# Kernel tuning notes

Measured on AMD Instinct MI355X. Metric: run time of the kernel, lower is better.

The kernel has to match this reference:

```python
import jax, jax.numpy as jnp
import numpy as np

S, E, K, D = 50000, 20000, 128, 64
NUM_LAYER = 3
E1, E0 = 1000000, 1000000  # nnz of pos / neg adjacency
B = 4096


def _edges(key, n_rows, n_cols, n_edges):
    k1, k2, k3 = jax.random.split(key, 3)
    rows = jax.random.randint(k1, (n_edges,), 0, n_rows)
    cols = jax.random.randint(k2, (n_edges,), 0, n_cols)
    vals = jax.random.uniform(k3, (n_edges,), jnp.float32, 0.0, 0.1)
    return rows, cols, vals


def setup_inputs() -> dict:
    key = jax.random.key(0)
    ks = jax.random.split(key, 32)
    inp = {}
    inp['stu_id'] = jax.random.randint(ks[0], (B,), 0, S)
    inp['exer_id'] = jax.random.randint(ks[1], (B,), 0, E)
    inp['kn_emb'] = (jax.random.uniform(ks[2], (B, K)) < 0.1).astype(jnp.float32)
    # embeddings
    inp['stu_emb'] = jax.random.normal(ks[3], (S, D), jnp.float32) * 0.1
    inp['exer_emb'] = jax.random.normal(ks[4], (E, D), jnp.float32) * 0.1
    inp['kn_base'] = jax.random.normal(ks[5], (K, D), jnp.float32) * 0.1
    inp['stu_bias'] = jax.random.normal(ks[6], (S, 1), jnp.float32) * 0.1
    inp['e_disc'] = jax.random.normal(ks[7], (E, 1), jnp.float32) * 0.1
    # GCN linear layers
    inp['W1_w'] = jax.random.normal(ks[8], (K, K), jnp.float32) * (1.0 / np.sqrt(K))
    inp['W1_b'] = jnp.zeros((K,), jnp.float32)
    inp['W0_w'] = jax.random.normal(ks[9], (K, K), jnp.float32) * (1.0 / np.sqrt(K))
    inp['W0_b'] = jnp.zeros((K,), jnp.float32)
    # PosLinear prednet
    inp['pn1_w'] = jax.random.normal(ks[10], (256, K), jnp.float32) * 0.05
    inp['pn1_b'] = jnp.zeros((256,), jnp.float32)
    inp['pn2_w'] = jax.random.normal(ks[11], (128, 256), jnp.float32) * 0.05
    inp['pn2_b'] = jnp.zeros((128,), jnp.float32)
    inp['pn3_w'] = jax.random.normal(ks[12], (1, 128), jnp.float32) * 0.05
    inp['pn3_b'] = jnp.zeros((1,), jnp.float32)
    # sparse adjacencies (COO) pos(1) / neg(0), user->item and item->user
    r, c, v = _edges(ks[13], S, E, E1)
    inp['ui1_r'], inp['ui1_c'], inp['ui1_v'] = r, c, v
    r, c, v = _edges(ks[14], E, S, E1)
    inp['iu1_r'], inp['iu1_c'], inp['iu1_v'] = r, c, v
    r, c, v = _edges(ks[15], S, E, E0)
    inp['ui0_r'], inp['ui0_c'], inp['ui0_v'] = r, c, v
    r, c, v = _edges(ks[16], E, S, E0)
    inp['iu0_r'], inp['iu0_c'], inp['iu0_v'] = r, c, v
    # self-loop degree normalizers (1/(deg+1)-style positive scalars)
    inp['d_i_1'] = jax.random.uniform(ks[17], (S,), jnp.float32, 0.01, 1.0)
    inp['d_j_1'] = jax.random.uniform(ks[18], (E,), jnp.float32, 0.01, 1.0)
    inp['d_i_0'] = jax.random.uniform(ks[19], (S,), jnp.float32, 0.01, 1.0)
    inp['d_j_0'] = jax.random.uniform(ks[20], (E,), jnp.float32, 0.01, 1.0)
    return inp


def _spmm(rows, cols, vals, x, n_rows):
    # sparse [n_rows, n_cols] @ dense [n_cols, K]
    return jax.ops.segment_sum(vals[:, None] * x[cols], rows, num_segments=n_rows)


def _poslinear(x, w, b):
    wp = 2.0 * jax.nn.relu(-w) + w  # == |w|, as in PosLinear
    return x @ wp.T + b


def reference(stu_id, exer_id, kn_emb, stu_emb, exer_emb, kn_base, stu_bias, e_disc,
              W1_w, W1_b, W0_w, W0_b, pn1_w, pn1_b, pn2_w, pn2_b, pn3_w, pn3_b,
              ui1_r, ui1_c, ui1_v, iu1_r, iu1_c, iu1_v,
              ui0_r, ui0_c, ui0_v, iu0_r, iu0_c, iu0_v,
              d_i_1, d_j_1, d_i_0, d_j_0):
    # project embeddings onto knowledge space: [S,K], [E,K]
    stat = stu_emb @ kn_base.T
    kdiff = exer_emb @ kn_base.T
    for _ in range(NUM_LAYER):
        u1 = _spmm(ui1_r, ui1_c, ui1_v, kdiff, S) + stat * d_i_1[:, None]
        u1 = u1 @ W1_w.T + W1_b
        i1 = _spmm(iu1_r, iu1_c, iu1_v, stat, E) + kdiff * d_j_1[:, None]
        i1 = i1 @ W1_w.T + W1_b
        u0 = _spmm(ui0_r, ui0_c, ui0_v, kdiff, S) + stat * d_i_0[:, None]
        u0 = u0 @ W0_w.T + W0_b
        i0 = _spmm(iu0_r, iu0_c, iu0_v, stat, E) + kdiff * d_j_0[:, None]
        i0 = i0 @ W0_w.T + W0_b
        stat = u1 + u0
        kdiff = i1 + i0
    # diagnosis head (NCD-style), dropout in eval mode -> identity
    stat_b = jax.nn.sigmoid(stat[stu_id] + stu_bias[stu_id])      # [B,K]
    k_d = jax.nn.sigmoid(kdiff[exer_id])                           # [B,K]
    disc = jax.nn.sigmoid(e_disc[exer_id])                         # [B,1]
    x = disc * (stat_b - k_d) * kn_emb
    x = jax.nn.sigmoid(_poslinear(x, pn1_w, pn1_b))
    x = jax.nn.sigmoid(_poslinear(x, pn2_w, pn2_b))
    out = jax.nn.sigmoid(_poslinear(x, pn3_w, pn3_b)).reshape(-1)
    return out
```

## Files before the change

### kernel.cpp

```cpp
#include <hip/hip_runtime.h>
#include <hip/hip_bf16.h>

#define SN 50000
#define EN 20000
#define KN 128
#define DN 64
#define BN 4096
#define NE 1000000
#define NLAYER 3

#define CH_SHIFT 12
#define NCH0 5
#define NCH1 13
#define SIDE1_BASE2 (2 * SN * NCH0)
#define NTOT2 (2 * (SN * NCH0 + EN * NCH1))

#define BIN_SHIFT 11
#define NBIN2 ((NTOT2 + 2047) >> 11)
#define T1 4096
#define PG1 ((NE + T1 - 1) / T1)
#define HB 256

typedef float f32x4 __attribute__((ext_vector_type(4)));
typedef float f32x2 __attribute__((ext_vector_type(2)));
typedef short bf16x8 __attribute__((ext_vector_type(8)));

__device__ __forceinline__ float sigmoidf_(float v) { return 1.f / (1.f + __expf(-v)); }
__device__ __forceinline__ float bf_lo(unsigned u) { return __uint_as_float(u << 16); }
__device__ __forceinline__ float bf_hi(unsigned u) { return __uint_as_float(u & 0xffff0000u); }
__device__ __forceinline__ float bf_one(unsigned short s) { return __uint_as_float((unsigned)s << 16); }
__device__ __forceinline__ unsigned packbf2(float a, float b) {
    __hip_bfloat16 ha = __float2bfloat16(a), hb = __float2bfloat16(b);
    unsigned short ua = *(unsigned short*)&ha, ub = *(unsigned short*)&hb;
    return (unsigned)ua | ((unsigned)ub << 16);
}
__device__ __forceinline__ unsigned short packbf1(float a) {
    __hip_bfloat16 ha = __float2bfloat16(a);
    return *(unsigned short*)&ha;
}
__device__ __forceinline__ unsigned char fp8_of_bf16(unsigned short h) {
    float f = bf_one(h);
    int pk = __builtin_amdgcn_cvt_pk_fp8_f32(f, f, 0, false);
    return (unsigned char)(pk & 0xff);
}

struct CsrB {
    const int* rows[4]; const int* cols[4]; const float* vals[4];
};

__device__ __forceinline__ int bucket_idx(int a, int r, int cc) {
    int side = a >> 1;
    int nch = side ? NCH1 : NCH0;
    int base = side ? SIDE1_BASE2 : 0;
    int tb = a & 1;
    return base + (2 * r + tb) * nch + (cc >> CH_SHIFT);
}

__global__ __launch_bounds__(256) void hist_coarse(CsrB c, int* __restrict__ cnt) {
    __shared__ int h[512];
    const int t = threadIdx.x;
    h[t] = 0; h[t + 256] = 0;
    __syncthreads();
    const int a = blockIdx.x >> 8;
    const int tile = blockIdx.x & 255;
    const int per = (NE + HB - 1) / HB;
    const int beg = tile * per, end = min(beg + per, NE);
    for (int i = beg + t; i < end; i += 256)
        atomicAdd(&h[bucket_idx(a, c.rows[a][i], c.cols[a][i]) >> BIN_SHIFT], 1);
    __syncthreads();
    if (h[t]) atomicAdd(&cnt[t], h[t]);
    if (h[t + 256]) atomicAdd(&cnt[t + 256], h[t + 256]);
}

__global__ __launch_bounds__(512) void scan_coarse(const int* __restrict__ cnt,
                                                   int* __restrict__ base,
                                                   int* __restrict__ tails) {
    __shared__ int sh[512];
    const int t = threadIdx.x;
    const int v = (t < NBIN2) ? cnt[t] : 0;
    sh[t] = v;
    __syncthreads();
    for (int o = 1; o < 512; o <<= 1) {
        int x = sh[t]; int u = (t >= o) ? sh[t - o] : 0;
        __syncthreads(); sh[t] = x + u; __syncthreads();
    }
    if (t < NBIN2) {
        const int ex = sh[t] - v;
        base[t] = ex;
        tails[t] = ex;
    }
    if (t == 511) base[NBIN2] = sh[511];
}

__global__ __launch_bounds__(512) void part1(CsrB c, int* __restrict__ tails,
                                             int2* __restrict__ stg) {
    __shared__ int2 srec[T1];
    __shared__ unsigned short sbin[T1];
    __shared__ int h[512], offs[512], gbase[512], sc[512];
    const int t = threadIdx.x;
    const int a = blockIdx.x / PG1;
    const int tile = blockIdx.x - a * PG1;
    const int beg = tile * T1;
    const int cnt = min(T1, NE - beg);
    h[t] = 0;
    __syncthreads();

    int2 rec[8]; int rbin[8]; int rrank[8];
#pragma unroll
    for (int k = 0; k < 8; ++k) {
        int o = t + k * 512;
        if (o < cnt) {
            int i = beg + o;
            int cc = c.cols[a][i];
            int B = bucket_idx(a, c.rows[a][i], cc);
            int bin = B >> BIN_SHIFT;
            rec[k] = make_int2(cc | ((B & 2047) << 17), __float_as_int(c.vals[a][i]));
            rbin[k] = bin;
            rrank[k] = atomicAdd(&h[bin], 1);
        } else {
            rbin[k] = -1;
        }
    }
    __syncthreads();
    sc[t] = h[t];
    __syncthreads();
    for (int o = 1; o < 512; o <<= 1) {
        int x = sc[t]; int u = (t >= o) ? sc[t - o] : 0;
        __syncthreads(); sc[t] = x + u; __syncthreads();
    }
    offs[t] = sc[t] - h[t];
    if (h[t] > 0) gbase[t] = atomicAdd(&tails[t], h[t]);
    __syncthreads();
#pragma unroll
    for (int k = 0; k < 8; ++k) {
        if (rbin[k] >= 0) {
            int pos = offs[rbin[k]] + rrank[k];
            srec[pos] = rec[k];
            sbin[pos] = (unsigned short)rbin[k];
        }
    }
    __syncthreads();
    for (int idx = t; idx < cnt; idx += 512) {
        int b = sbin[idx];
        stg[gbase[b] + (idx - offs[b])] = srec[idx];
    }
}

__global__ __launch_bounds__(512) void part2(const int* __restrict__ coarseBase,
                                             const int2* __restrict__ stg,
                                             int* __restrict__ rp,
                                             int2* __restrict__ cv) {
    __shared__ int cnt2[2048];
    __shared__ int tsum[512];
    const int b = blockIdx.x;
    const int t = threadIdx.x;
    const int fineBase = b << BIN_SHIFT;
    const int nf = min(2048, NTOT2 - fineBase);
    const int segBeg = coarseBase[b];
    const int segEnd = coarseBase[b + 1];
    for (int i = t; i < 2048; i += 512) cnt2[i] = 0;
    __syncthreads();
    for (int e = segBeg + t; e < segEnd; e += 512)
        atomicAdd(&cnt2[((unsigned)stg[e].x) >> 17], 1);
    __syncthreads();
    const int i4 = t * 4;
    int v0 = cnt2[i4], v1 = cnt2[i4 + 1], v2 = cnt2[i4 + 2], v3 = cnt2[i4 + 3];
    tsum[t] = v0 + v1 + v2 + v3;
    __syncthreads();
    for (int o = 1; o < 512; o <<= 1) {
        int x = tsum[t]; int u = (t >= o) ? tsum[t - o] : 0;
        __syncthreads(); tsum[t] = x + u; __syncthreads();
    }
    const int pre = (t == 0) ? 0 : tsum[t - 1];
    const int p0 = pre, p1 = pre + v0, p2 = p1 + v1, p3 = p2 + v2;
    cnt2[i4] = p0; cnt2[i4 + 1] = p1; cnt2[i4 + 2] = p2; cnt2[i4 + 3] = p3;
    if (i4 + 0 < nf) rp[fineBase + i4 + 0] = segBeg + p0;
    if (i4 + 1 < nf) rp[fineBase + i4 + 1] = segBeg + p1;
    if (i4 + 2 < nf) rp[fineBase + i4 + 2] = segBeg + p2;
    if (i4 + 3 < nf) rp[fineBase + i4 + 3] = segBeg + p3;
    if (b == NBIN2 - 1 && t == 511) rp[NTOT2] = segEnd;
    __syncthreads();
    for (int e = segBeg + t; e < segEnd; e += 512) {
        int2 r = stg[e];
        int pos = segBeg + atomicAdd(&cnt2[((unsigned)r.x) >> 17], 1);
        cv[pos] = make_int2(r.x & 0xFFFF, r.y);
    }
}

__global__ __launch_bounds__(256) void f2bf3(
    const float* __restrict__ s0, unsigned short* __restrict__ d0, int n0,
    const float* __restrict__ s1, unsigned short* __restrict__ d1, int n1,
    const float* __restrict__ s2, unsigned short* __restrict__ d2, int n2) {
    int j = blockIdx.x * 256 + threadIdx.x;
    const float* s; unsigned short* d;
    if (j < n0) { s = s0; d = d0; }
    else {
        j -= n0;
        if (j < n1) { s = s1; d = d1; }
        else {
            j -= n1;
            if (j >= n2) return;
            s = s2; d = d2;
        }
    }
    float2 f = ((const float2*)s)[j];
    ((unsigned*)d)[j] = packbf2(f.x, f.y);
}

template <int KK>
__global__ __launch_bounds__(256) void gemm_proj(const float* __restrict__ X,
                                                 const unsigned short* __restrict__ W,
                                                 unsigned short* __restrict__ out,
                                                 unsigned char* __restrict__ f8,
                                                 int M) {
    constexpr int PITCH = KK + 8;
    __shared__ unsigned short Wl[128 * PITCH];
    const int t = threadIdx.x;
    for (int idx = t * 8; idx < 128 * KK; idx += 2048) {
        int r = idx / KK, k = idx - r * KK;
        *(uint4*)(&Wl[r * PITCH + k]) = *(const uint4*)(&W[idx]);
    }
    __syncthreads();
    const int lane = t & 63;
    const int nm = lane & 15;
    const int quad = lane >> 4;
    const int row0 = blockIdx.x * 64 + (t >> 6) * 16;
    if (row0 >= M) return;

    f32x4 acc[8];
#pragma unroll
    for (int nt = 0; nt < 8; ++nt) acc[nt] = (f32x4){0.f, 0.f, 0.f, 0.f};

    const float* xrow = X + (size_t)(row0 + nm) * KK + quad * 8;
#pragma unroll
    for (int ks = 0; ks < KK / 32; ++ks) {
        float4 f0 = *(const float4*)(xrow + ks * 32);
        float4 f1 = *(const float4*)(xrow + ks * 32 + 4);
        unsigned q[4] = {packbf2(f0.x, f0.y), packbf2(f0.z, f0.w),
                         packbf2(f1.x, f1.y), packbf2(f1.z, f1.w)};
        bf16x8 a = *(bf16x8*)q;
#pragma unroll
        for (int nt = 0; nt < 8; ++nt) {
            bf16x8 b = *(const bf16x8*)(&Wl[(nt * 16 + nm) * PITCH + ks * 32 + quad * 8]);
            acc[nt] = __builtin_amdgcn_mfma_f32_16x16x32_bf16(a, b, acc[nt], 0, 0, 0);
        }
    }
    const size_t obase = (size_t)(row0 + quad * 4) * 128 + nm;
    unsigned short* orow = out + obase;
    unsigned char* frow = f8 + obase;
#pragma unroll
    for (int r = 0; r < 4; ++r)
#pragma unroll
        for (int nt = 0; nt < 8; ++nt) {
            unsigned short h = packbf1(acc[nt][r]);
            orow[(size_t)r * 128 + nt * 16] = h;
            frow[(size_t)r * 128 + nt * 16] = fp8_of_bf16(h);
        }
}

template <bool LIST>
__global__ __launch_bounds__(512) void gemm2_mfma(
    const unsigned short* __restrict__ agg1S, const unsigned short* __restrict__ agg0S,
    const unsigned short* __restrict__ yS,
    const float* __restrict__ d1S, const float* __restrict__ d0S,
    unsigned short* __restrict__ outS, unsigned char* __restrict__ f8S,
    const unsigned short* __restrict__ agg1E, const unsigned short* __restrict__ agg0E,
    const unsigned short* __restrict__ yE,
    const float* __restrict__ d1E, const float* __restrict__ d0E,
    unsigned short* __restrict__ outE, unsigned char* __restrict__ f8E,
    const unsigned short* __restrict__ W1, const unsigned short* __restrict__ W0,
    const float* __restrict__ b1, const float* __restrict__ b0,
    const int* __restrict__ idsS, const int* __restrict__ idsE, int nblkS) {
    constexpr int PITCH = 136;
    __shared__ unsigned short Wl[2 * 128 * PITCH];
    const int t = threadIdx.x;
    for (int idx = t * 8; idx < 128 * 128; idx += 4096) {
        int r = idx >> 7, k = idx & 127;
        *(uint4*)(&Wl[r * PITCH + k]) = *(const uint4*)(&W1[idx]);
        *(uint4*)(&Wl[128 * PITCH + r * PITCH + k]) = *(const uint4*)(&W0[idx]);
    }
    __syncthreads();
    const bool sideE = (int)blockIdx.x >= nblkS;
    const unsigned short* agg1 = sideE ? agg1E : agg1S;
    const unsigned short* agg0 = sideE ? agg0E : agg0S;
    const unsigned short* y    = sideE ? yE : yS;
    const float* d1 = sideE ? d1E : d1S;
    const float* d0 = sideE ? d0E : d0S;
    unsigned short* out = sideE ? outE : outS;
    unsigned char* f8 = sideE ? f8E : f8S;
    const int M = LIST ? BN : (sideE ? EN : SN);
    const int lane = t & 63;
    const int nm = lane & 15;
    const int quad = lane >> 4;
    const int row0 = ((int)blockIdx.x - (sideE ? nblkS : 0)) * 128 + (t >> 6) * 16;
    if (row0 >= M) return;

    const int lrow = row0 + nm;
    int grow = lrow;
    if (LIST) grow = (sideE ? idsE : idsS)[lrow];

    const float d1v = d1[grow];
    const float d0v = d0[grow];

    f32x4 acc[8];
#pragma unroll
    for (int nt = 0; nt < 8; ++nt) acc[nt] = (f32x4){0.f, 0.f, 0.f, 0.f};

    const size_t rbA = (size_t)lrow * 128 + quad * 8;
    const size_t rbY = (size_t)grow * 128 + quad * 8;
#pragma unroll
    for (int ks = 0; ks < 4; ++ks) {
        uint4 ua1 = *(const uint4*)(agg1 + rbA + ks * 32);
        uint4 ua0 = *(const uint4*)(agg0 + rbA + ks * 32);
        uint4 uy  = *(const uint4*)(y    + rbY + ks * 32);
        uint4 p1, p0;
        {
            unsigned* a1 = (unsigned*)&ua1; unsigned* a0 = (unsigned*)&ua0;
            unsigned* yy = (unsigned*)&uy;
            unsigned* q1 = (unsigned*)&p1; unsigned* q0 = (unsigned*)&p0;
#pragma unroll
            for (int w = 0; w < 4; ++w) {
                float ylo = bf_lo(yy[w]), yhi = bf_hi(yy[w]);
                q1[w] = packbf2(bf_lo(a1[w]) + d1v * ylo, bf_hi(a1[w]) + d1v * yhi);
                q0[w] = packbf2(bf_lo(a0[w]) + d0v * ylo, bf_hi(a0[w]) + d0v * yhi);
            }
        }
        bf16x8 af1 = *(bf16x8*)&p1;
        bf16x8 af0 = *(bf16x8*)&p0;
#pragma unroll
        for (int nt = 0; nt < 8; ++nt) {
            bf16x8 bw1 = *(const bf16x8*)(&Wl[(nt * 16 + nm) * PITCH + ks * 32 + quad * 8]);
            acc[nt] = __builtin_amdgcn_mfma_f32_16x16x32_bf16(af1, bw1, acc[nt], 0, 0, 0);
            bf16x8 bw0 = *(const bf16x8*)(&Wl[128 * PITCH + (nt * 16 + nm) * PITCH + ks * 32 + quad * 8]);
            acc[nt] = __builtin_amdgcn_mfma_f32_16x16x32_bf16(af0, bw0, acc[nt], 0, 0, 0);
        }
    }
    const size_t obase = (size_t)(row0 + quad * 4) * 128 + nm;
    unsigned short* orow = out + obase;
    unsigned char* frow = f8 + obase;
#pragma unroll
    for (int nt = 0; nt < 8; ++nt) {
        float bb = b1[nt * 16 + nm] + b0[nt * 16 + nm];
#pragma unroll
        for (int r = 0; r < 4; ++r) {
            unsigned short h = packbf1(acc[nt][r] + bb);
            orow[(size_t)r * 128 + nt * 16] = h;
            if (!LIST) frow[(size_t)r * 128 + nt * 16] = fp8_of_bf16(h);
        }
    }
}

template <bool LIST>
__global__ __launch_bounds__(256) void spmm_all(
    const int* __restrict__ rp, const long long* __restrict__ cv,
    const unsigned char* __restrict__ kd8, const unsigned char* __restrict__ st8,
    unsigned short* __restrict__ as1, unsigned short* __restrict__ as0,
    unsigned short* __restrict__ ae1, unsigned short* __restrict__ ae0,
    const int* __restrict__ idsS, const int* __restrict__ idsE) {
    const int wave = (blockIdx.x * 256 + threadIdx.x) >> 6;
    const int lane = threadIdx.x & 63;
    const int NW = LIST ? 2 * BN : SN + EN;
    if (wave >= NW) return;
    const bool sideE = LIST ? (wave >= BN) : (wave >= SN);
    const int li = sideE ? (wave - (LIST ? BN : SN)) : wave;
    const int r = LIST ? (sideE ? idsE[li] : idsS[li]) : li;
    const int nch = sideE ? NCH1 : NCH0;
    const int* rpb = rp + (sideE ? SIDE1_BASE2 : 0);
    const int o = lane >> 3;
    const int c = lane & 7;
    const unsigned char* g8 = (sideE ? st8 : kd8) + c * 16;

    const int rbase = 2 * r * nch;
    const int e0 = rpb[rbase];
    const int em = rpb[rbase + nch];
    const int ee = rpb[rbase + 2 * nch];

    f32x2 acc[8];

#define OCT(E)                                                              \
    {                                                                       \
        int col = (int)((E) & 0xFFFF);                                      \
        float v = __int_as_float((int)((E) >> 32));                         \
        f32x2 vv = {v, v};                                                  \
        uint4 u = *(const uint4*)(g8 + (col << 7));                         \
        acc[0] += vv * __builtin_amdgcn_cvt_pk_f32_fp8((int)u.x, false);    \
        acc[1] += vv * __builtin_amdgcn_cvt_pk_f32_fp8((int)u.x, true);     \
        acc[2] += vv * __builtin_amdgcn_cvt_pk_f32_fp8((int)u.y, false);    \
        acc[3] += vv * __builtin_amdgcn_cvt_pk_f32_fp8((int)u.y, true);     \
        acc[4] += vv * __builtin_amdgcn_cvt_pk_f32_fp8((int)u.z, false);    \
        acc[5] += vv * __builtin_amdgcn_cvt_pk_f32_fp8((int)u.z, true);     \
        acc[6] += vv * __builtin_amdgcn_cvt_pk_f32_fp8((int)u.w, false);    \
        acc[7] += vv * __builtin_amdgcn_cvt_pk_f32_fp8((int)u.w, true);     \
    }

#define PHASE(EBEG, EEND)                                                   \
    {                                                                       \
        int e = (EBEG);                                                     \
        for (; e + 16 <= (EEND); e += 16) {                                 \
            long long E0 = cv[e + o];                                       \
            long long E1 = cv[e + 8 + o];                                   \
            OCT(E0) OCT(E1)                                                 \
        }                                                                   \
        for (; e + 8 <= (EEND); e += 8) {                                   \
            long long E0 = cv[e + o];                                       \
            OCT(E0)                                                         \
        }                                                                   \
        if (e < (EEND)) {                                                   \
            int idx = min(e + o, (EEND) - 1);                               \
            long long E0 = cv[idx];                                         \
            if (e + o >= (EEND)) E0 &= 0xFFFFLL;    \
            OCT(E0)                                                         \
        }                                                                   \
    }

#define REDUCE8                                                             \
    _Pragma("unroll")                                                       \
    for (int j = 0; j < 8; ++j) {                                           \
        acc[j].x += __shfl_xor(acc[j].x, 8);                                \
        acc[j].y += __shfl_xor(acc[j].y, 8);                                \
        acc[j].x += __shfl_xor(acc[j].x, 16);                               \
        acc[j].y += __shfl_xor(acc[j].y, 16);                               \
        acc[j].x += __shfl_xor(acc[j].x, 32);                               \
        acc[j].y += __shfl_xor(acc[j].y, 32);                               \
    }

    const int oi = LIST ? li : r;
    const int base = (oi << 7) + c * 16;
    unsigned short* o1 = sideE ? ae1 : as1;
    unsigned short* o0 = sideE ? ae0 : as0;

#pragma unroll
    for (int j = 0; j < 8; ++j) acc[j] = (f32x2){0.f, 0.f};
    PHASE(e0, em)
    REDUCE8
    if (o == 0) {
        uint4 w1, w2;
        w1.x = packbf2(acc[0].x, acc[0].y); w1.y = packbf2(acc[1].x, acc[1].y);
        w1.z = packbf2(acc[2].x, acc[2].y); w1.w = packbf2(acc[3].x, acc[3].y);
        w2.x = packbf2(acc[4].x, acc[4].y); w2.y = packbf2(acc[5].x, acc[5].y);
        w2.z = packbf2(acc[6].x, acc[6].y); w2.w = packbf2(acc[7].x, acc[7].y);
        *(uint4*)&o1[base] = w1;
        *(uint4*)&o1[base + 8] = w2;
    }

#pragma unroll
    for (int j = 0; j < 8; ++j) acc[j] = (f32x2){0.f, 0.f};
    PHASE(em, ee)
    REDUCE8
    if (o == 1) {
        uint4 w1, w2;
        w1.x = packbf2(acc[0].x, acc[0].y); w1.y = packbf2(acc[1].x, acc[1].y);
        w1.z = packbf2(acc[2].x, acc[2].y); w1.w = packbf2(acc[3].x, acc[3].y);
        w2.x = packbf2(acc[4].x, acc[4].y); w2.y = packbf2(acc[5].x, acc[5].y);
        w2.z = packbf2(acc[6].x, acc[6].y); w2.w = packbf2(acc[7].x, acc[7].y);
        *(uint4*)&o0[base] = w1;
        *(uint4*)&o0[base + 8] = w2;
    }
#undef OCT
#undef PHASE
#undef REDUCE8
}

template <int KK, int NCOLS, int ROWS, bool ABSW, bool SIG>
__global__ __launch_bounds__(256) void gemm_xwT(const float* __restrict__ X,
                                                const float* __restrict__ W,
                                                const float* __restrict__ bias,
                                                float* __restrict__ out, int M) {
    constexpr int KP = 32;
    constexpr int NG = 256 / NCOLS;
    constexpr int RT = ROWS / NG;
    __shared__ float BT[KP * (NCOLS + 1)];
    __shared__ float Xl[ROWS * (KK + 1)];
    const int t = threadIdx.x;
    const int j = t % NCOLS;
    const int rg = t / NCOLS;
    const int row0 = blockIdx.x * ROWS;

    for (int idx = t; idx < ROWS * KK; idx += 256) {
        int r = idx / KK, k = idx % KK;
        int gr = row0 + r;
        Xl[r * (KK + 1) + k] = (gr < M) ? X[gr * KK + k] : 0.f;
    }
    float acc[RT];
#pragma unroll
    for (int i = 0; i < RT; ++i) acc[i] = 0.f;

    for (int k0 = 0; k0 < KK; k0 += KP) {
        __syncthreads();
        for (int idx = t; idx < NCOLS * KP; idx += 256) {
            int jj = idx / KP, kp = idx % KP;
            float w = W[jj * KK + k0 + kp];
            BT[kp * (NCOLS + 1) + jj] = ABSW ? fabsf(w) : w;
        }
        __syncthreads();
#pragma unroll
        for (int kp = 0; kp < KP; ++kp) {
            float b = BT[kp * (NCOLS + 1) + j];
#pragma unroll
            for (int rr = 0; rr < RT; ++rr)
                acc[rr] += Xl[(rg * RT + rr) * (KK + 1) + k0 + kp] * b;
        }
    }
    float bj = bias ? bias[j] : 0.f;
#pragma unroll
    for (int rr = 0; rr < RT; ++rr) {
        int gr = row0 + rg * RT + rr;
        if (gr < M) {
            float v = acc[rr] + bj;
            out[gr * NCOLS + j] = SIG ? sigmoidf_(v) : v;
        }
    }
}

__global__ __launch_bounds__(128) void head1_kernel(
    const int* __restrict__ stu_id, const int* __restrict__ exer_id,
    const float* __restrict__ kn_emb, const unsigned short* __restrict__ statB,
    const unsigned short* __restrict__ kdB, const float* __restrict__ stu_bias,
    const float* __restrict__ e_disc, float* __restrict__ x) {
    const int b = blockIdx.x;
    const int k = threadIdx.x;
    const int sid = stu_id[b], eid = exer_id[b];
    float disc = sigmoidf_(e_disc[eid]);
    float sb = sigmoidf_(bf_one(statB[(b << 7) + k]) + stu_bias[sid]);
    float kd = sigmoidf_(bf_one(kdB[(b << 7) + k]));
    x[(b << 7) + k] = disc * (sb - kd) * kn_emb[(b << 7) + k];
}

__global__ __launch_bounds__(256) void pn3_kernel(const float* __restrict__ h2,
                                                  const float* __restrict__ w3,
                                                  const float* __restrict__ b3,
                                                  float* __restrict__ out) {
    __shared__ float wl[128];
    const int t = threadIdx.x;
    if (t < 128) wl[t] = fabsf(w3[t]);
    __syncthreads();
    const int b = blockIdx.x * 256 + t;
    float acc = 0.f;
#pragma unroll 4
    for (int k = 0; k < 128; ++k) acc += h2[(b << 7) + k] * wl[k];
    out[b] = sigmoidf_(acc + b3[0]);
}

static inline size_t align256(size_t x) { return (x + 255) & ~size_t(255); }

extern "C" void kernel_launch(void* const* d_in, const int* in_sizes, int n_in,
                              void* d_out, int out_size, void* d_ws, size_t ws_size,
                              hipStream_t stream) {
    const int*   stu_id   = (const int*)d_in[0];
    const int*   exer_id  = (const int*)d_in[1];
    const float* kn_emb   = (const float*)d_in[2];
    const float* stu_emb  = (const float*)d_in[3];
    const float* exer_emb = (const float*)d_in[4];
    const float* kn_base  = (const float*)d_in[5];
    const float* stu_bias = (const float*)d_in[6];
    const float* e_disc   = (const float*)d_in[7];
    const float* W1_w     = (const float*)d_in[8];
    const float* W1_b     = (const float*)d_in[9];
    const float* W0_w     = (const float*)d_in[10];
    const float* W0_b     = (const float*)d_in[11];
    const float* pn1_w    = (const float*)d_in[12];
    const float* pn1_b    = (const float*)d_in[13];
    const float* pn2_w    = (const float*)d_in[14];
    const float* pn2_b    = (const float*)d_in[15];
    const float* pn3_w    = (const float*)d_in[16];
    const float* pn3_b    = (const float*)d_in[17];
    const int*   ui1_r = (const int*)d_in[18]; const int* ui1_c = (const int*)d_in[19];
    const float* ui1_v = (const float*)d_in[20];
    const int*   iu1_r = (const int*)d_in[21]; const int* iu1_c = (const int*)d_in[22];
    const float* iu1_v = (const float*)d_in[23];
    const int*   ui0_r = (const int*)d_in[24]; const int* ui0_c = (const int*)d_in[25];
    const float* ui0_v = (const float*)d_in[26];
    const int*   iu0_r = (const int*)d_in[27]; const int* iu0_c = (const int*)d_in[28];
    const float* iu0_v = (const float*)d_in[29];
    const float* d_i_1 = (const float*)d_in[30];
    const float* d_j_1 = (const float*)d_in[31];
    const float* d_i_0 = (const float*)d_in[32];
    const float* d_j_0 = (const float*)d_in[33];
    float* out = (float*)d_out;

    typedef unsigned short u16;
    typedef unsigned char u8;
    char* p = (char*)d_ws;
    size_t off = 0;
    auto alloc = [&](size_t bytes) { char* q = p + off; off += align256(bytes); return q; };
    u16* stat  = (u16*)alloc(size_t(SN) * KN * 2);
    u16* kdiff = (u16*)alloc(size_t(EN) * KN * 2);
    u8* st8 = (u8*)alloc(size_t(SN) * KN);
    u8* kd8 = (u8*)alloc(size_t(EN) * KN);
    u16* as1 = (u16*)alloc(size_t(SN) * KN * 2);
    u16* as0 = (u16*)alloc(size_t(SN) * KN * 2);
    u16* ae1 = (u16*)alloc(size_t(EN) * KN * 2);
    u16* ae0 = (u16*)alloc(size_t(EN) * KN * 2);
    u16* statB = (u16*)alloc(size_t(BN) * KN * 2);
    u16* kdB   = (u16*)alloc(size_t(BN) * KN * 2);
    u16* Kb  = (u16*)alloc(size_t(KN) * DN * 2);
    u16* Wb1 = (u16*)alloc(size_t(KN) * KN * 2);
    u16* Wb0 = (u16*)alloc(size_t(KN) * KN * 2);
    int*  coarseCnt  = (int*)alloc(512 * 4);
    int*  coarseBase = (int*)alloc((NBIN2 + 1) * 4);
    int*  tails      = (int*)alloc(512 * 4);
    int*  rp_all     = (int*)alloc(size_t(NTOT2 + 1) * 4);
    int2* stg        = (int2*)alloc(size_t(4) * NE * 8);
    int2* cv_all     = (int2*)alloc(size_t(4) * NE * 8);
    float* xh = (float*)alloc(size_t(BN) * KN * 4);
    float* h1 = (float*)alloc(size_t(BN) * 256 * 4);
    float* h2 = (float*)alloc(size_t(BN) * 128 * 4);
    if (off > ws_size) return;

    CsrB c;
    c.rows[0] = ui1_r; c.cols[0] = ui1_c; c.vals[0] = ui1_v;
    c.rows[1] = ui0_r; c.cols[1] = ui0_c; c.vals[1] = ui0_v;
    c.rows[2] = iu1_r; c.cols[2] = iu1_c; c.vals[2] = iu1_v;
    c.rows[3] = iu0_r; c.cols[3] = iu0_c; c.vals[3] = iu0_v;

    hipMemsetAsync(coarseCnt, 0, 512 * 4, stream);
    hist_coarse<<<4 * HB, 256, 0, stream>>>(c, coarseCnt);
    scan_coarse<<<1, 512, 0, stream>>>(coarseCnt, coarseBase, tails);
    part1<<<4 * PG1, 512, 0, stream>>>(c, tails, stg);
    part2<<<NBIN2, 512, 0, stream>>>(coarseBase, stg, rp_all, cv_all);

    {
        const int n0 = KN * DN / 2, n1 = KN * KN / 2, n2 = KN * KN / 2;
        f2bf3<<<(n0 + n1 + n2 + 255) / 256, 256, 0, stream>>>(
            kn_base, Kb, n0, W1_w, Wb1, n1, W0_w, Wb0, n2);
    }

    gemm_proj<DN><<<(SN + 63) / 64, 256, 0, stream>>>(stu_emb, Kb, stat, st8, SN);
    gemm_proj<DN><<<(EN + 63) / 64, 256, 0, stream>>>(exer_emb, Kb, kdiff, kd8, EN);

    const int nblkS = (SN + 127) / 128, nblkE = (EN + 127) / 128;

    for (int l = 0; l < NLAYER; ++l) {
        if (l < NLAYER - 1) {
            spmm_all<false><<<(SN + EN + 3) / 4, 256, 0, stream>>>(
                rp_all, (const long long*)cv_all, kd8, st8, as1, as0, ae1, ae0,
                nullptr, nullptr);
            gemm2_mfma<false><<<nblkS + nblkE, 512, 0, stream>>>(
                as1, as0, stat, d_i_1, d_i_0, stat, st8,
                ae1, ae0, kdiff, d_j_1, d_j_0, kdiff, kd8,
                Wb1, Wb0, W1_b, W0_b, nullptr, nullptr, nblkS);
        } else {
            spmm_all<true><<<(2 * BN) / 4, 256, 0, stream>>>(
                rp_all, (const long long*)cv_all, kd8, st8, as1, as0, ae1, ae0,
                stu_id, exer_id);
            gemm2_mfma<true><<<2 * (BN / 128), 512, 0, stream>>>(
                as1, as0, stat, d_i_1, d_i_0, statB, nullptr,
                ae1, ae0, kdiff, d_j_1, d_j_0, kdB, nullptr,
                Wb1, Wb0, W1_b, W0_b, stu_id, exer_id, BN / 128);
        }
    }

    head1_kernel<<<BN, 128, 0, stream>>>(stu_id, exer_id, kn_emb, statB, kdB,
                                         stu_bias, e_disc, xh);
    gemm_xwT<128, 256, 16, true, true><<<BN / 16, 256, 0, stream>>>(xh, pn1_w, pn1_b, h1, BN);
    gemm_xwT<256, 128, 32, true, true><<<BN / 32, 256, 0, stream>>>(h1, pn2_w, pn2_b, h2, BN);
    pn3_kernel<<<BN / 256, 256, 0, stream>>>(h2, pn3_w, pn3_b, out);
    (void)out_size; (void)n_in; (void)in_sizes;
}
```

Measured before the change: 611.1 us.

## Process four rows per wave in SpMM with 16 lanes per row

Restructures the SpMM so each 64-lane wave handles four output rows, with 16 lanes per row each loading 8 fp8 columns, instead of one row per wave with 8 edges in flight. Each lane group walks its row's edges sequentially, using a common-minimum unrolled loop plus a masked tail, so the cross-lane reduction shuffles are gone. The intent is to remove reduction overhead and to waste fewer lanes on short rows. The cost is divergence when row lengths differ within a wave and less edge-level parallelism per row.

```diff
diff --git a/kernel.cpp b/kernel.cpp
--- a/kernel.cpp
+++ b/kernel.cpp
@@ -359,106 +359,88 @@
     const int* __restrict__ idsS, const int* __restrict__ idsE) {
     const int wave = (blockIdx.x * 256 + threadIdx.x) >> 6;
     const int lane = threadIdx.x & 63;
-    const int NW = LIST ? 2 * BN : SN + EN;
+    const int q = lane >> 4;
+    const int c = lane & 15;
+    const int NW = LIST ? (2 * BN / 4) : ((SN + EN) / 4);
     if (wave >= NW) return;
-    const bool sideE = LIST ? (wave >= BN) : (wave >= SN);
-    const int li = sideE ? (wave - (LIST ? BN : SN)) : wave;
-    const int r = LIST ? (sideE ? idsE[li] : idsS[li]) : li;
+    const bool sideE = LIST ? (wave >= BN / 4) : (wave >= SN / 4);
+    const int wb = wave - (sideE ? (LIST ? BN / 4 : SN / 4) : 0);
+    const int li = wb * 4 + q;
+    const int r = LIST ? ((sideE ? idsE : idsS)[li]) : li;
     const int nch = sideE ? NCH1 : NCH0;
     const int* rpb = rp + (sideE ? SIDE1_BASE2 : 0);
-    const int o = lane >> 3;
-    const int c = lane & 7;
-    const unsigned char* g8 = (sideE ? st8 : kd8) + c * 16;
+    const unsigned char* g8 = (sideE ? st8 : kd8) + c * 8;
 
     const int rbase = 2 * r * nch;
-    const int e0 = rpb[rbase];
+    int e        = rpb[rbase];
     const int em = rpb[rbase + nch];
     const int ee = rpb[rbase + 2 * nch];
 
-    f32x2 acc[8];
-
-#define OCT(E)                                                              \
+    f32x2 acc[4];
+
+#define GQUAD(E)                                                            \
     {                                                                       \
         int col = (int)((E) & 0xFFFF);                                      \
         float v = __int_as_float((int)((E) >> 32));                         \
         f32x2 vv = {v, v};                                                  \
-        uint4 u = *(const uint4*)(g8 + (col << 7));                         \
+        uint2 u = *(const uint2*)(g8 + (col << 7));                         \
         acc[0] += vv * __builtin_amdgcn_cvt_pk_f32_fp8((int)u.x, false);    \
         acc[1] += vv * __builtin_amdgcn_cvt_pk_f32_fp8((int)u.x, true);     \
         acc[2] += vv * __builtin_amdgcn_cvt_pk_f32_fp8((int)u.y, false);    \
         acc[3] += vv * __builtin_amdgcn_cvt_pk_f32_fp8((int)u.y, true);     \
-        acc[4] += vv * __builtin_amdgcn_cvt_pk_f32_fp8((int)u.z, false);    \
-        acc[5] += vv * __builtin_amdgcn_cvt_pk_f32_fp8((int)u.z, true);     \
-        acc[6] += vv * __builtin_amdgcn_cvt_pk_f32_fp8((int)u.w, false);    \
-        acc[7] += vv * __builtin_amdgcn_cvt_pk_f32_fp8((int)u.w, true);     \
-    }
-
-#define PHASE(EBEG, EEND)                                                   \
+    }
+
+#define RUNPHASE(EEND)                                                      \
     {                                                                       \
-        int e = (EBEG);                                                     \
-        for (; e + 16 <= (EEND); e += 16) {                                 \
-            long long E0 = cv[e + o];                                       \
-            long long E1 = cv[e + 8 + o];                                   \
-            OCT(E0) OCT(E1)                                                 \
+        int len = (EEND) - e;                                               \
+        int mn = min(len, __shfl_xor(len, 16));                             \
+        mn = min(mn, __shfl_xor(mn, 32));                                   \
+        const int eCom = e + (mn & ~3);                                     \
+        for (; e < eCom; e += 4) {                                          \
+            long long E0 = cv[e];                                           \
+            long long E1 = cv[e + 1];                                       \
+            long long E2 = cv[e + 2];                                       \
+            long long E3 = cv[e + 3];                                       \
+            GQUAD(E0) GQUAD(E1) GQUAD(E2) GQUAD(E3)                         \
         }                                                                   \
-        for (; e + 8 <= (EEND); e += 8) {                                   \
-            long long E0 = cv[e + o];                                       \
-            OCT(E0)                                                         \
+        while (__any(e < (EEND))) {                                         \
+            int idx = max(min(e, (EEND) - 1), 0);                           \
+            long long E0 = cv[idx];                                         \
+            if (e >= (EEND)) E0 &= 0xFFFFLL;   \
+            GQUAD(E0)                                                       \
+            ++e;                                                            \
         }                                                                   \
-        if (e < (EEND)) {                                                   \
-            int idx = min(e + o, (EEND) - 1);                               \
-            long long E0 = cv[idx];                                         \
-            if (e + o >= (EEND)) E0 &= 0xFFFFLL;    \
-            OCT(E0)                                                         \
-        }                                                                   \
-    }
-
-#define REDUCE8                                                             \
-    _Pragma("unroll")                                                       \
-    for (int j = 0; j < 8; ++j) {                                           \
-        acc[j].x += __shfl_xor(acc[j].x, 8);                                \
-        acc[j].y += __shfl_xor(acc[j].y, 8);                                \
-        acc[j].x += __shfl_xor(acc[j].x, 16);                               \
-        acc[j].y += __shfl_xor(acc[j].y, 16);                               \
-        acc[j].x += __shfl_xor(acc[j].x, 32);                               \
-        acc[j].y += __shfl_xor(acc[j].y, 32);                               \
     }
 
     const int oi = LIST ? li : r;
-    const int base = (oi << 7) + c * 16;
-    unsigned short* o1 = sideE ? ae1 : as1;
-    unsigned short* o0 = sideE ? ae0 : as0;
-
-#pragma unroll
-    for (int j = 0; j < 8; ++j) acc[j] = (f32x2){0.f, 0.f};
-    PHASE(e0, em)
-    REDUCE8
-    if (o == 0) {
-        uint4 w1, w2;
-        w1.x = packbf2(acc[0].x, acc[0].y); w1.y = packbf2(acc[1].x, acc[1].y);
-        w1.z = packbf2(acc[2].x, acc[2].y); w1.w = packbf2(acc[3].x, acc[3].y);
-        w2.x = packbf2(acc[4].x, acc[4].y); w2.y = packbf2(acc[5].x, acc[5].y);
-        w2.z = packbf2(acc[6].x, acc[6].y); w2.w = packbf2(acc[7].x, acc[7].y);
-        *(uint4*)&o1[base] = w1;
-        *(uint4*)&o1[base + 8] = w2;
-    }
-
-#pragma unroll
-    for (int j = 0; j < 8; ++j) acc[j] = (f32x2){0.f, 0.f};
-    PHASE(em, ee)
-    REDUCE8
-    if (o == 1) {
-        uint4 w1, w2;
-        w1.x = packbf2(acc[0].x, acc[0].y); w1.y = packbf2(acc[1].x, acc[1].y);
-        w1.z = packbf2(acc[2].x, acc[2].y); w1.w = packbf2(acc[3].x, acc[3].y);
-        w2.x = packbf2(acc[4].x, acc[4].y); w2.y = packbf2(acc[5].x, acc[5].y);
-        w2.z = packbf2(acc[6].x, acc[6].y); w2.w = packbf2(acc[7].x, acc[7].y);
-        *(uint4*)&o0[base] = w1;
-        *(uint4*)&o0[base + 8] = w2;
-    }
-#undef OCT
-#undef PHASE
-#undef REDUCE8
+    const int base = (oi << 7) + c * 8;
+
+#pragma unroll
+    for (int j = 0; j < 4; ++j) acc[j] = (f32x2){0.f, 0.f};
+    RUNPHASE(em)
+    {
+        uint4 w;
+        w.x = packbf2(acc[0].x, acc[0].y);
+        w.y = packbf2(acc[1].x, acc[1].y);
+        w.z = packbf2(acc[2].x, acc[2].y);
+        w.w = packbf2(acc[3].x, acc[3].y);
+        *(uint4*)&(sideE ? ae1 : as1)[base] = w;
+    }
+
+    e = em;
+#pragma unroll
+    for (int j = 0; j < 4; ++j) acc[j] = (f32x2){0.f, 0.f};
+    RUNPHASE(ee)
+    {
+        uint4 w;
+        w.x = packbf2(acc[0].x, acc[0].y);
+        w.y = packbf2(acc[1].x, acc[1].y);
+        w.z = packbf2(acc[2].x, acc[2].y);
+        w.w = packbf2(acc[3].x, acc[3].y);
+        *(uint4*)&(sideE ? ae0 : as0)[base] = w;
+    }
+#undef GQUAD
+#undef RUNPHASE
 }
 
 template <int KK, int NCOLS, int ROWS, bool ABSW, bool SIG>
@@ -632,7 +614,7 @@
 
     for (int l = 0; l < NLAYER; ++l) {
         if (l < NLAYER - 1) {
-            spmm_all<false><<<(SN + EN + 3) / 4, 256, 0, stream>>>(
+            spmm_all<false><<<(SN + EN) / 16, 256, 0, stream>>>(
                 rp_all, (const long long*)cv_all, kd8, st8, as1, as0, ae1, ae0,
                 nullptr, nullptr);
             gemm2_mfma<false><<<nblkS + nblkE, 512, 0, stream>>>(
@@ -640,7 +622,7 @@
                 ae1, ae0, kdiff, d_j_1, d_j_0, kdiff, kd8,
                 Wb1, Wb0, W1_b, W0_b, nullptr, nullptr, nblkS);
         } else {
-            spmm_all<true><<<(2 * BN) / 4, 256, 0, stream>>>(
+            spmm_all<true><<<(2 * BN) / 16, 256, 0, stream>>>(
                 rp_all, (const long long*)cv_all, kd8, st8, as1, as0, ae1, ae0,
                 stu_id, exer_id);
             gemm2_mfma<true><<<2 * (BN / 128), 512, 0, stream>>>(
```

After: 661.4 us. 8.2% more time.
